# Kernel optimization log

Hardware: AMD Instinct MI355X
Metric: run time of the kernel (lower is better)

## Reference

```python
import jax, jax.numpy as jnp
import numpy as np

EPS = 1e-8


def setup_inputs() -> dict:
    key = jax.random.key(0)
    k1, k2, k3, k4 = jax.random.split(key, 4)
    B, N, M, C = 512, 512, 128, 1024
    addr = M + 6  # read head: k(M) + beta(1) + g(1) + s(3) + gamma(1)
    controller_out = jax.random.normal(k1, (B, C), dtype=jnp.float32)
    prev_w = jax.random.uniform(k2, (B, N), dtype=jnp.float32)
    prev_w = prev_w / prev_w.sum(axis=1, keepdims=True)  # valid weighting
    memory_state = jax.random.normal(k3, (B, N, M), dtype=jnp.float32)
    W_fc = jax.random.normal(k4, (C, addr), dtype=jnp.float32) * 0.02
    b_fc = jnp.zeros((addr,), dtype=jnp.float32)
    return {"controller_out": controller_out, "prev_w": prev_w,
            "memory_state": memory_state, "W_fc": W_fc, "b_fc": b_fc}


def reference(controller_out, prev_w, memory_state, W_fc, b_fc):
    M = memory_state.shape[2]
    out = controller_out @ W_fc + b_fc  # [B, M+6]
    k = out[:, :M]                                   # key
    beta = jax.nn.softplus(out[:, M:M + 1])          # key strength
    g = jax.nn.sigmoid(out[:, M + 1:M + 2])          # interpolation gate
    s = jax.nn.softmax(out[:, M + 2:M + 5], axis=1)  # 3-tap shift weights
    gamma = 1.0 + jax.nn.softplus(out[:, M + 5:M + 6])

    # Content addressing (Eq. 5-6): cosine similarity + sharpened softmax
    norm_k = jnp.linalg.norm(k, axis=1, keepdims=True) + EPS      # [B,1]
    norm_mem = jnp.linalg.norm(memory_state, axis=2) + EPS        # [B,N]
    sim = jnp.einsum('bnm,bm->bn', memory_state, k) / (norm_k * norm_mem)
    w_c = jax.nn.softmax(beta * sim, axis=1)

    # Interpolation (Eq. 7)
    w_g = g * w_c + (1.0 - g) * prev_w

    # Circular 3-tap shift (Eq. 8): vectorized roll instead of per-slot loop
    w_s = (s[:, 0:1] * jnp.roll(w_g, 1, axis=1)
           + s[:, 1:2] * w_g
           + s[:, 2:3] * jnp.roll(w_g, -1, axis=1))

    # Sharpening (Eq. 9)
    w_pow = w_s ** gamma
    w = w_pow / (w_pow.sum(axis=1, keepdims=True) + EPS)

    # Read vector (read head)
    read_vec = jnp.einsum('bn,bnm->bm', w, memory_state)
    return (read_vec, w)
```

## Files before the change

kernel.cpp:

```cpp
#include <hip/hip_runtime.h>
#include <math.h>

#define BB   512
#define NN   512
#define MM   128
#define CC   1024
#define ADDR 134
#define EPSF 1e-8f

__device__ __forceinline__ float softplus_f(float x) {
    return fmaxf(x, 0.0f) + log1pf(expf(-fabsf(x)));
}

__global__ __launch_bounds__(256) void ntm_head_kernel(
    const float* __restrict__ co,
    const float* __restrict__ prev_w,
    const float* __restrict__ mem,
    const float* __restrict__ W_fc,
    const float* __restrict__ b_fc,
    float* __restrict__ out_rv,
    float* __restrict__ out_w)
{
    __shared__ __align__(16) float s_co[CC];
    __shared__ __align__(16) float s_k[MM];
    __shared__ float s_extra[8];
    __shared__ float s_bsim[NN];
    __shared__ float s_wg[NN];
    __shared__ float s_w[NN];
    __shared__ __align__(16) float s_part[8 * MM];
    __shared__ float s_red[8];
    __shared__ float s_params[8];

    const int t = threadIdx.x;
    const int b = blockIdx.x;

    for (int c = t; c < CC; c += 256) s_co[c] = co[(size_t)b * CC + c];
    __syncthreads();

    if (t < ADDR) {
        float a0 = 0.f, a1 = 0.f, a2 = 0.f, a3 = 0.f;
        const float* Wp = W_fc + t;
        for (int c = 0; c < CC; c += 4) {
            float4 cv = *(const float4*)(s_co + c);
            a0 = fmaf(cv.x, Wp[(size_t)(c + 0) * ADDR], a0);
            a1 = fmaf(cv.y, Wp[(size_t)(c + 1) * ADDR], a1);
            a2 = fmaf(cv.z, Wp[(size_t)(c + 2) * ADDR], a2);
            a3 = fmaf(cv.w, Wp[(size_t)(c + 3) * ADDR], a3);
        }
        float r = ((a0 + a1) + (a2 + a3)) + b_fc[t];
        if (t < MM) s_k[t] = r; else s_extra[t - MM] = r;
    }
    __syncthreads();

    {
        float v = (t < MM) ? s_k[t] * s_k[t] : 0.0f;
        #pragma unroll
        for (int off = 32; off >= 1; off >>= 1) v += __shfl_xor(v, off, 64);
        if ((t & 63) == 0) s_red[t >> 6] = v;
        __syncthreads();
        if (t == 0) {
            float ks = s_red[0] + s_red[1] + s_red[2] + s_red[3];
            float norm_k = sqrtf(ks) + EPSF;
            float beta = softplus_f(s_extra[0]);
            float g = 1.0f / (1.0f + expf(-s_extra[1]));
            float e0 = s_extra[2], e1 = s_extra[3], e2 = s_extra[4];
            float mx = fmaxf(e0, fmaxf(e1, e2));
            float x0 = expf(e0 - mx), x1 = expf(e1 - mx), x2 = expf(e2 - mx);
            float inv = 1.0f / (x0 + x1 + x2);
            s_params[0] = beta / norm_k;
            s_params[1] = g;
            s_params[2] = x0 * inv;
            s_params[3] = x1 * inv;
            s_params[4] = x2 * inv;
            s_params[5] = 1.0f + softplus_f(s_extra[5]);
        }
    }
    __syncthreads();

    const float bnk = s_params[0];
    const float4* memb = (const float4*)(mem + (size_t)b * NN * MM);

    {
        const int gi = t >> 5;
        const int l  = t & 31;
        float4 kv = ((const float4*)s_k)[l];
        for (int n0 = gi; n0 < NN; n0 += 32) {
            float4 a0 = memb[(size_t)(n0     ) * 32 + l];
            float4 a1 = memb[(size_t)(n0 +  8) * 32 + l];
            float4 a2 = memb[(size_t)(n0 + 16) * 32 + l];
            float4 a3 = memb[(size_t)(n0 + 24) * 32 + l];
            float d0 = a0.x*kv.x + a0.y*kv.y + a0.z*kv.z + a0.w*kv.w;
            float q0 = a0.x*a0.x + a0.y*a0.y + a0.z*a0.z + a0.w*a0.w;
            float d1 = a1.x*kv.x + a1.y*kv.y + a1.z*kv.z + a1.w*kv.w;
            float q1 = a1.x*a1.x + a1.y*a1.y + a1.z*a1.z + a1.w*a1.w;
            float d2 = a2.x*kv.x + a2.y*kv.y + a2.z*kv.z + a2.w*kv.w;
            float q2 = a2.x*a2.x + a2.y*a2.y + a2.z*a2.z + a2.w*a2.w;
            float d3 = a3.x*kv.x + a3.y*kv.y + a3.z*kv.z + a3.w*kv.w;
            float q3 = a3.x*a3.x + a3.y*a3.y + a3.z*a3.z + a3.w*a3.w;
            #pragma unroll
            for (int off = 16; off >= 1; off >>= 1) {
                d0 += __shfl_xor(d0, off, 64); q0 += __shfl_xor(q0, off, 64);
                d1 += __shfl_xor(d1, off, 64); q1 += __shfl_xor(q1, off, 64);
                d2 += __shfl_xor(d2, off, 64); q2 += __shfl_xor(q2, off, 64);
                d3 += __shfl_xor(d3, off, 64); q3 += __shfl_xor(q3, off, 64);
            }
            if (l == 0) {
                s_bsim[n0     ] = bnk * d0 / (sqrtf(q0) + EPSF);
                s_bsim[n0 +  8] = bnk * d1 / (sqrtf(q1) + EPSF);
                s_bsim[n0 + 16] = bnk * d2 / (sqrtf(q2) + EPSF);
                s_bsim[n0 + 24] = bnk * d3 / (sqrtf(q3) + EPSF);
            }
        }
    }
    __syncthreads();

    {
        const int n1 = t, n2 = t + 256;
        float b1 = s_bsim[n1], b2 = s_bsim[n2];

        float m = fmaxf(b1, b2);
        #pragma unroll
        for (int off = 32; off >= 1; off >>= 1) m = fmaxf(m, __shfl_xor(m, off, 64));
        if ((t & 63) == 0) s_red[t >> 6] = m;
        __syncthreads();
        float M4 = fmaxf(fmaxf(s_red[0], s_red[1]), fmaxf(s_red[2], s_red[3]));
        __syncthreads();

        float e1 = expf(b1 - M4), e2 = expf(b2 - M4);
        float ls = e1 + e2;
        #pragma unroll
        for (int off = 32; off >= 1; off >>= 1) ls += __shfl_xor(ls, off, 64);
        if ((t & 63) == 0) s_red[t >> 6] = ls;
        __syncthreads();
        float S = s_red[0] + s_red[1] + s_red[2] + s_red[3];
        __syncthreads();

        const float invS = 1.0f / S;
        const float g = s_params[1];
        float wg1 = fmaf(g, e1 * invS, (1.0f - g) * prev_w[(size_t)b * NN + n1]);
        float wg2 = fmaf(g, e2 * invS, (1.0f - g) * prev_w[(size_t)b * NN + n2]);
        s_wg[n1] = wg1;
        s_wg[n2] = wg2;
        __syncthreads();

        const float sh0 = s_params[2], sh1 = s_params[3], sh2 = s_params[4];
        const float gamma = s_params[5];
        float ws1 = sh0 * s_wg[(n1 + NN - 1) & (NN - 1)] + sh1 * wg1 + sh2 * s_wg[(n1 + 1) & (NN - 1)];
        float ws2 = sh0 * s_wg[(n2 + NN - 1) & (NN - 1)] + sh1 * wg2 + sh2 * s_wg[(n2 + 1) & (NN - 1)];
        float wp1 = powf(ws1, gamma);
        float wp2 = powf(ws2, gamma);

        float lz = wp1 + wp2;
        #pragma unroll
        for (int off = 32; off >= 1; off >>= 1) lz += __shfl_xor(lz, off, 64);
        if ((t & 63) == 0) s_red[t >> 6] = lz;
        __syncthreads();
        float Z = s_red[0] + s_red[1] + s_red[2] + s_red[3];
        __syncthreads();

        const float invZ = 1.0f / (Z + EPSF);
        float w1 = wp1 * invZ, w2 = wp2 * invZ;
        s_w[n1] = w1;
        s_w[n2] = w2;
        out_w[(size_t)b * NN + n1] = w1;
        out_w[(size_t)b * NN + n2] = w2;
    }
    __syncthreads();

    {
        const int q = t >> 5;
        const int l = t & 31;
        float4 acc = make_float4(0.f, 0.f, 0.f, 0.f);
        const int nb = q * 64;
        for (int n = nb; n < nb + 64; n += 4) {
            float4 a0 = memb[(size_t)(n    ) * 32 + l];
            float4 a1 = memb[(size_t)(n + 1) * 32 + l];
            float4 a2 = memb[(size_t)(n + 2) * 32 + l];
            float4 a3 = memb[(size_t)(n + 3) * 32 + l];
            float w0 = s_w[n], w1 = s_w[n + 1], w2 = s_w[n + 2], w3 = s_w[n + 3];
            acc.x = fmaf(w0, a0.x, acc.x); acc.y = fmaf(w0, a0.y, acc.y);
            acc.z = fmaf(w0, a0.z, acc.z); acc.w = fmaf(w0, a0.w, acc.w);
            acc.x = fmaf(w1, a1.x, acc.x); acc.y = fmaf(w1, a1.y, acc.y);
            acc.z = fmaf(w1, a1.z, acc.z); acc.w = fmaf(w1, a1.w, acc.w);
            acc.x = fmaf(w2, a2.x, acc.x); acc.y = fmaf(w2, a2.y, acc.y);
            acc.z = fmaf(w2, a2.z, acc.z); acc.w = fmaf(w2, a2.w, acc.w);
            acc.x = fmaf(w3, a3.x, acc.x); acc.y = fmaf(w3, a3.y, acc.y);
            acc.z = fmaf(w3, a3.z, acc.z); acc.w = fmaf(w3, a3.w, acc.w);
        }
        *((float4*)&s_part[q * MM + l * 4]) = acc;
        __syncthreads();
        if (t < MM) {
            float r = 0.f;
            #pragma unroll
            for (int q2 = 0; q2 < 8; ++q2) r += s_part[q2 * MM + t];
            out_rv[(size_t)b * MM + t] = r;
        }
    }
}

extern "C" void kernel_launch(void* const* d_in, const int* in_sizes, int n_in,
                              void* d_out, int out_size, void* d_ws, size_t ws_size,
                              hipStream_t stream) {
    const float* co     = (const float*)d_in[0];
    const float* prev_w = (const float*)d_in[1];
    const float* mem    = (const float*)d_in[2];
    const float* W_fc   = (const float*)d_in[3];
    const float* b_fc   = (const float*)d_in[4];
    float* out = (float*)d_out;
    ntm_head_kernel<<<BB, 256, 0, stream>>>(co, prev_w, mem, W_fc, b_fc,
                                            out, out + (size_t)BB * MM);
}
```

Before: 239.6 us.

## Use 1024-thread blocks and split FC reduction across four thread groups

Raises the block size from 256 to 1024 threads. The controller FC projection is split into four partial K-ranges reduced through shared memory, and the memory similarity and read passes are redistributed over more waves. This targets the latency-bound serial FC loop and the low per-block parallelism. In exchange, 1024-thread blocks limit scheduling granularity and add more partial sums to reduce.

```diff
diff --git a/kernel.cpp b/kernel.cpp
--- a/kernel.cpp
+++ b/kernel.cpp
@@ -7,12 +7,13 @@
 #define CC   1024
 #define ADDR 134
 #define EPSF 1e-8f
+#define NT   1024
 
 __device__ __forceinline__ float softplus_f(float x) {
     return fmaxf(x, 0.0f) + log1pf(expf(-fabsf(x)));
 }
 
-__global__ __launch_bounds__(256) void ntm_head_kernel(
+__global__ __launch_bounds__(NT) void ntm_head_kernel(
     const float* __restrict__ co,
     const float* __restrict__ prev_w,
     const float* __restrict__ mem,
@@ -24,30 +25,42 @@
     __shared__ __align__(16) float s_co[CC];
     __shared__ __align__(16) float s_k[MM];
     __shared__ float s_extra[8];
+    __shared__ float s_fcpart[4 * ADDR];
     __shared__ float s_bsim[NN];
     __shared__ float s_wg[NN];
     __shared__ float s_w[NN];
-    __shared__ __align__(16) float s_part[8 * MM];
-    __shared__ float s_red[8];
+    __shared__ __align__(16) float s_part[32 * MM];
+    __shared__ float s_red[16];
     __shared__ float s_params[8];
 
     const int t = threadIdx.x;
     const int b = blockIdx.x;
-
-    for (int c = t; c < CC; c += 256) s_co[c] = co[(size_t)b * CC + c];
-    __syncthreads();
-
+    const int wv = t >> 6;
+
+    s_co[t] = co[(size_t)b * CC + t];
+    __syncthreads();
+
+    {
+        const int q = t >> 8;
+        const int j = t & 255;
+        if (j < ADDR) {
+            float a0 = 0.f, a1 = 0.f, a2 = 0.f, a3 = 0.f;
+            const float* Wp = W_fc + j;
+            const int c0 = q * 256;
+            for (int c = c0; c < c0 + 256; c += 4) {
+                float4 cv = *(const float4*)(s_co + c);
+                a0 = fmaf(cv.x, Wp[(size_t)(c + 0) * ADDR], a0);
+                a1 = fmaf(cv.y, Wp[(size_t)(c + 1) * ADDR], a1);
+                a2 = fmaf(cv.z, Wp[(size_t)(c + 2) * ADDR], a2);
+                a3 = fmaf(cv.w, Wp[(size_t)(c + 3) * ADDR], a3);
+            }
+            s_fcpart[q * ADDR + j] = (a0 + a1) + (a2 + a3);
+        }
+    }
+    __syncthreads();
     if (t < ADDR) {
-        float a0 = 0.f, a1 = 0.f, a2 = 0.f, a3 = 0.f;
-        const float* Wp = W_fc + t;
-        for (int c = 0; c < CC; c += 4) {
-            float4 cv = *(const float4*)(s_co + c);
-            a0 = fmaf(cv.x, Wp[(size_t)(c + 0) * ADDR], a0);
-            a1 = fmaf(cv.y, Wp[(size_t)(c + 1) * ADDR], a1);
-            a2 = fmaf(cv.z, Wp[(size_t)(c + 2) * ADDR], a2);
-            a3 = fmaf(cv.w, Wp[(size_t)(c + 3) * ADDR], a3);
-        }
-        float r = ((a0 + a1) + (a2 + a3)) + b_fc[t];
+        float r = s_fcpart[t] + s_fcpart[ADDR + t] + s_fcpart[2 * ADDR + t]
+                + s_fcpart[3 * ADDR + t] + b_fc[t];
         if (t < MM) s_k[t] = r; else s_extra[t - MM] = r;
     }
     __syncthreads();
@@ -56,10 +69,12 @@
         float v = (t < MM) ? s_k[t] * s_k[t] : 0.0f;
         #pragma unroll
         for (int off = 32; off >= 1; off >>= 1) v += __shfl_xor(v, off, 64);
-        if ((t & 63) == 0) s_red[t >> 6] = v;
+        if ((t & 63) == 0) s_red[wv] = v;
         __syncthreads();
         if (t == 0) {
-            float ks = s_red[0] + s_red[1] + s_red[2] + s_red[3];
+            float ks = 0.f;
+            #pragma unroll
+            for (int i = 0; i < 16; ++i) ks += s_red[i];
             float norm_k = sqrtf(ks) + EPSF;
             float beta = softplus_f(s_extra[0]);
             float g = 1.0f / (1.0f + expf(-s_extra[1]));
@@ -84,11 +99,11 @@
         const int gi = t >> 5;
         const int l  = t & 31;
         float4 kv = ((const float4*)s_k)[l];
-        for (int n0 = gi; n0 < NN; n0 += 32) {
-            float4 a0 = memb[(size_t)(n0     ) * 32 + l];
-            float4 a1 = memb[(size_t)(n0 +  8) * 32 + l];
-            float4 a2 = memb[(size_t)(n0 + 16) * 32 + l];
-            float4 a3 = memb[(size_t)(n0 + 24) * 32 + l];
+        for (int n0 = gi; n0 < NN; n0 += 128) {
+            float4 a0 = memb[(size_t)(n0      ) * 32 + l];
+            float4 a1 = memb[(size_t)(n0 + 32 ) * 32 + l];
+            float4 a2 = memb[(size_t)(n0 + 64 ) * 32 + l];
+            float4 a3 = memb[(size_t)(n0 + 96 ) * 32 + l];
             float d0 = a0.x*kv.x + a0.y*kv.y + a0.z*kv.z + a0.w*kv.w;
             float q0 = a0.x*a0.x + a0.y*a0.y + a0.z*a0.z + a0.w*a0.w;
             float d1 = a1.x*kv.x + a1.y*kv.y + a1.z*kv.z + a1.w*kv.w;
@@ -105,65 +120,70 @@
                 d3 += __shfl_xor(d3, off, 64); q3 += __shfl_xor(q3, off, 64);
             }
             if (l == 0) {
-                s_bsim[n0     ] = bnk * d0 / (sqrtf(q0) + EPSF);
-                s_bsim[n0 +  8] = bnk * d1 / (sqrtf(q1) + EPSF);
-                s_bsim[n0 + 16] = bnk * d2 / (sqrtf(q2) + EPSF);
-                s_bsim[n0 + 24] = bnk * d3 / (sqrtf(q3) + EPSF);
+                s_bsim[n0      ] = bnk * d0 / (sqrtf(q0) + EPSF);
+                s_bsim[n0 + 32 ] = bnk * d1 / (sqrtf(q1) + EPSF);
+                s_bsim[n0 + 64 ] = bnk * d2 / (sqrtf(q2) + EPSF);
+                s_bsim[n0 + 96 ] = bnk * d3 / (sqrtf(q3) + EPSF);
             }
         }
     }
     __syncthreads();
 
     {
-        const int n1 = t, n2 = t + 256;
-        float b1 = s_bsim[n1], b2 = s_bsim[n2];
-
-        float m = fmaxf(b1, b2);
+        const bool act = (t < NN);
+        float bv = act ? s_bsim[t] : -INFINITY;
+        float pw = act ? prev_w[(size_t)b * NN + t] : 0.0f;
+
+        float m = bv;
         #pragma unroll
         for (int off = 32; off >= 1; off >>= 1) m = fmaxf(m, __shfl_xor(m, off, 64));
-        if ((t & 63) == 0) s_red[t >> 6] = m;
-        __syncthreads();
-        float M4 = fmaxf(fmaxf(s_red[0], s_red[1]), fmaxf(s_red[2], s_red[3]));
-        __syncthreads();
-
-        float e1 = expf(b1 - M4), e2 = expf(b2 - M4);
-        float ls = e1 + e2;
+        if ((t & 63) == 0) s_red[wv] = m;
+        __syncthreads();
+        float M8 = -INFINITY;
+        #pragma unroll
+        for (int i = 0; i < 8; ++i) M8 = fmaxf(M8, s_red[i]);
+        __syncthreads();
+
+        float e = act ? expf(bv - M8) : 0.0f;
+        float ls = e;
         #pragma unroll
         for (int off = 32; off >= 1; off >>= 1) ls += __shfl_xor(ls, off, 64);
-        if ((t & 63) == 0) s_red[t >> 6] = ls;
-        __syncthreads();
-        float S = s_red[0] + s_red[1] + s_red[2] + s_red[3];
+        if ((t & 63) == 0) s_red[wv] = ls;
+        __syncthreads();
+        float S = 0.f;
+        #pragma unroll
+        for (int i = 0; i < 16; ++i) S += s_red[i];
         __syncthreads();
 
         const float invS = 1.0f / S;
         const float g = s_params[1];
-        float wg1 = fmaf(g, e1 * invS, (1.0f - g) * prev_w[(size_t)b * NN + n1]);
-        float wg2 = fmaf(g, e2 * invS, (1.0f - g) * prev_w[(size_t)b * NN + n2]);
-        s_wg[n1] = wg1;
-        s_wg[n2] = wg2;
+        float wg = fmaf(g, e * invS, (1.0f - g) * pw);
+        if (act) s_wg[t] = wg;
         __syncthreads();
 
         const float sh0 = s_params[2], sh1 = s_params[3], sh2 = s_params[4];
         const float gamma = s_params[5];
-        float ws1 = sh0 * s_wg[(n1 + NN - 1) & (NN - 1)] + sh1 * wg1 + sh2 * s_wg[(n1 + 1) & (NN - 1)];
-        float ws2 = sh0 * s_wg[(n2 + NN - 1) & (NN - 1)] + sh1 * wg2 + sh2 * s_wg[(n2 + 1) & (NN - 1)];
-        float wp1 = powf(ws1, gamma);
-        float wp2 = powf(ws2, gamma);
-
-        float lz = wp1 + wp2;
+        float wp = 0.0f;
+        if (act) {
+            float ws = sh0 * s_wg[(t + NN - 1) & (NN - 1)] + sh1 * wg
+                     + sh2 * s_wg[(t + 1) & (NN - 1)];
+            wp = powf(ws, gamma);
+        }
+        float lz = wp;
         #pragma unroll
         for (int off = 32; off >= 1; off >>= 1) lz += __shfl_xor(lz, off, 64);
-        if ((t & 63) == 0) s_red[t >> 6] = lz;
-        __syncthreads();
-        float Z = s_red[0] + s_red[1] + s_red[2] + s_red[3];
-        __syncthreads();
+        if ((t & 63) == 0) s_red[wv] = lz;
+        __syncthreads();
+        float Z = 0.f;
+        #pragma unroll
+        for (int i = 0; i < 16; ++i) Z += s_red[i];
 
         const float invZ = 1.0f / (Z + EPSF);
-        float w1 = wp1 * invZ, w2 = wp2 * invZ;
-        s_w[n1] = w1;
-        s_w[n2] = w2;
-        out_w[(size_t)b * NN + n1] = w1;
-        out_w[(size_t)b * NN + n2] = w2;
+        if (act) {
+            float w = wp * invZ;
+            s_w[t] = w;
+            out_w[(size_t)b * NN + t] = w;
+        }
     }
     __syncthreads();
 
@@ -171,8 +191,10 @@
         const int q = t >> 5;
         const int l = t & 31;
         float4 acc = make_float4(0.f, 0.f, 0.f, 0.f);
-        const int nb = q * 64;
-        for (int n = nb; n < nb + 64; n += 4) {
+        const int nb = q * 16;
+        #pragma unroll
+        for (int i = 0; i < 16; i += 4) {
+            const int n = nb + i;
             float4 a0 = memb[(size_t)(n    ) * 32 + l];
             float4 a1 = memb[(size_t)(n + 1) * 32 + l];
             float4 a2 = memb[(size_t)(n + 2) * 32 + l];
@@ -192,7 +214,7 @@
         if (t < MM) {
             float r = 0.f;
             #pragma unroll
-            for (int q2 = 0; q2 < 8; ++q2) r += s_part[q2 * MM + t];
+            for (int q2 = 0; q2 < 32; ++q2) r += s_part[q2 * MM + t];
             out_rv[(size_t)b * MM + t] = r;
         }
     }
@@ -207,6 +229,6 @@
     const float* W_fc   = (const float*)d_in[3];
     const float* b_fc   = (const float*)d_in[4];
     float* out = (float*)d_out;
-    ntm_head_kernel<<<BB, 256, 0, stream>>>(co, prev_w, mem, W_fc, b_fc,
-                                            out, out + (size_t)BB * MM);
+    ntm_head_kernel<<<BB, NT, 0, stream>>>(co, prev_w, mem, W_fc, b_fc,
+                                           out, out + (size_t)BB * MM);
 }
```

Measured after the change: 245.9 us. +2.6%, slower.
